# Optimization experiments

Measured on AMD Instinct MI355X. Metric: run time of the kernel, lower is better.

The kernel has to match this reference:

```python
import jax, jax.numpy as jnp
import numpy as np

N_SIN = 3  # fcn_n_sin

def _feats(x):
    # x: [B, Din] -> features [B, Din, 1 + 2*N_SIN]
    omega = (2.0 ** jnp.arange(N_SIN, dtype=x.dtype))  # [n_sin]
    ox = x[..., None] * omega  # [B, Din, n_sin]
    return jnp.concatenate([x[..., None], jnp.sin(ox), jnp.cos(ox)], axis=-1)

def setup_inputs() -> dict:
    key = jax.random.key(0)
    k1, k2, k3 = jax.random.split(key, 3)
    B, Din, Dout, H, F = 2048, 64, 64, 32, 1 + 2 * N_SIN
    x = jax.random.normal(k1, (B, Din), dtype=jnp.float32)
    # xavier-normal-ish init for W1/W2, zeros for biases (matches init_parameters)
    W1 = jax.random.normal(k2, (Din, Dout, H, F), dtype=jnp.float32) * np.sqrt(2.0 / (H + F))
    W2 = jax.random.normal(k3, (Din, Dout, 1, H), dtype=jnp.float32) * np.sqrt(2.0 / (1 + H))
    B1 = jnp.zeros((Din, Dout, H), dtype=jnp.float32)
    B2 = jnp.zeros((Din, Dout, 1), dtype=jnp.float32)
    return {"x": x, "W1": W1, "W2": W2, "B1": B1, "B2": B2}

def reference(x, W1, W2, B1, B2):
    f = _feats(x)  # [B, Din, F]
    # per-edge first layer: [B, Din, Dout, H]
    h = jnp.einsum('bif,iohf->bioh', f, W1) + B1[None]
    h = jax.nn.silu(h)
    # per-edge second layer -> scalar: [B, Din, Dout]
    phis = jnp.einsum('bioh,ioh->bio', h, W2[:, :, 0, :]) + B2[:, :, 0][None]
    return phis.sum(axis=1)  # [B, Dout]
```

## Files before the change

kernel.cpp:

```cpp
#include <hip/hip_runtime.h>
#include <math.h>

typedef _Float16 f16;
typedef f16   f16x8    __attribute__((ext_vector_type(8)));
typedef float floatx4  __attribute__((ext_vector_type(4)));
typedef float floatx16 __attribute__((ext_vector_type(16)));

#define LOG2E 1.44269504088896340736f

#define B_SZ  2048
#define DIN   64
#define DOUT  64
#define NH    32

#define NIG   2
#define IGW   (DIN / NIG)

#define W1IMG_ELEMS ((size_t)DIN * DOUT * 64 * 8)
#define FIMG_ELEMS  ((size_t)DIN * 64 * 64 * 8)
#define W2Q_ELEMS   ((size_t)DIN * DOUT * NH)

__global__ __launch_bounds__(256) void prep_kernel(
        const float* __restrict__ W1, const float* __restrict__ B1,
        const float* __restrict__ W2, const float* __restrict__ B2,
        const float* __restrict__ x,
        f16* __restrict__ w1img, f16* __restrict__ fimg,
        float* __restrict__ w2q, float* __restrict__ b2sum) {
    const int bid = blockIdx.x, tid = threadIdx.x;
    if (bid < 256) {
        __shared__ float l1[16 * 225];
        __shared__ float lb[16 * 32];
        const int base = bid * 16;
        for (int g = tid; g < 3584; g += 256) {
            int pair = g / 224, r = g % 224;
            l1[pair * 225 + r] = W1[(size_t)base * 224 + g];
        }
        for (int g = tid; g < 512; g += 256) lb[g] = B1[(size_t)base * 32 + g];
        __syncthreads();
        for (int g = tid; g < 1024; g += 256) {
            int pair = g >> 6, lane = g & 63;
            f16x8 v = {};
            if (lane < 32) {
#pragma unroll
                for (int j = 0; j < 7; ++j)
                    v[j] = (f16)(l1[pair * 225 + lane * 7 + j] * (-LOG2E));
                v[7] = (f16)(lb[pair * 32 + lane] * (-LOG2E));
            }
            *(f16x8*)(w1img + (size_t)bid * 8192 + (size_t)g * 8) = v;
        }
    } else if (bid < 320) {
        __shared__ float ls[32 * 65];
        const int btp = bid - 256;
        for (int g = tid; g < 2048; g += 256) {
            int bb = g >> 6, i = g & 63;
            ls[bb * 65 + i] = x[(size_t)(btp * 32 + bb) * 64 + i];
        }
        __syncthreads();
        for (int g = tid; g < 2048; g += 256) {
            int bb = g & 31, i = g >> 5;
            float xv = ls[bb * 65 + i];
            float s1, c1;
            __sincosf(xv, &s1, &c1);
            float s2 = 2.0f * s1 * c1, c2 = 1.0f - 2.0f * s1 * s1;
            float s4 = 2.0f * s2 * c2, c4 = 1.0f - 2.0f * s2 * s2;
            f16x8 v;
            v[0] = (f16)xv; v[1] = (f16)s1; v[2] = (f16)s2; v[3] = (f16)s4;
            v[4] = (f16)c1; v[5] = (f16)c2; v[6] = (f16)c4; v[7] = (f16)1.0f;
            *(f16x8*)(fimg + ((size_t)(i * 64 + btp) * 64 + bb) * 8) = v;
        }
    } else if (bid < 832) {
        int e = (bid - 320) * 256 + tid;
        int r = e & 3, p = (e >> 2) & 1, q = (e >> 3) & 3;
        int o = (e >> 5) & 63, i = e >> 11;
        int h = q * 8 + p * 4 + r;
        w2q[e] = W2[(size_t)(i * 64 + o) * 32 + h] * (-1.0f / LOG2E);
    } else if (tid < 64) {
        float s = 0.0f;
        for (int i = 0; i < 64; ++i) s += B2[i * 64 + tid];
        b2sum[tid] = s;
    }
}

__global__ __launch_bounds__(128, 4) void main_kernel(
        const f16* __restrict__ w1img, const f16* __restrict__ fimg,
        const float* __restrict__ w2q, float* __restrict__ partials) {
    const int tid  = threadIdx.x;
    const int lane = tid & 63;
    const int wv   = tid >> 6;
    const int btp  = blockIdx.x & 63;
    const int og   = (blockIdx.x >> 6) & 31;
    const int ig   = blockIdx.x >> 11;
    const int o    = __builtin_amdgcn_readfirstlane(og * 2 + wv);
    const int p    = lane >> 5;

    const size_t ibase = (size_t)ig * IGW;
    const f16*   ap = w1img + ibase * 32768 + ((size_t)o * 64 + lane) * 8;
    const f16*   bp = fimg  + ibase * 32768 + ((size_t)btp * 64 + lane) * 8;
    const float* wp = w2q   + ibase * 2048  + (size_t)o * 32 + p * 4;

    f16x8 a = *(const f16x8*)ap;
    f16x8 b = *(const f16x8*)bp;

    float phi = 0.0f;
    const floatx16 zeroC = {};

#pragma unroll 1
    for (int ii = 0; ii < IGW; ++ii) {
        const f16x8 ca = a, cb = b;

        const size_t i1 = (size_t)(ii + 1);
        a = *(const f16x8*)(ap + i1 * 32768);
        b = *(const f16x8*)(bp + i1 * 32768);

        const floatx4 w0 = *(const floatx4*)(wp + (size_t)ii * 2048);
        const floatx4 w1 = *(const floatx4*)(wp + (size_t)ii * 2048 + 8);
        const floatx4 w2 = *(const floatx4*)(wp + (size_t)ii * 2048 + 16);
        const floatx4 w3 = *(const floatx4*)(wp + (size_t)ii * 2048 + 24);

        floatx16 C = __builtin_amdgcn_mfma_f32_32x32x16_f16(ca, cb, zeroC, 0, 0, 0);

#pragma unroll
        for (int q = 0; q < 4; ++q) {
            const floatx4 wq = (q == 0) ? w0 : (q == 1) ? w1 : (q == 2) ? w2 : w3;
            float t0 = C[4 * q + 0], t1 = C[4 * q + 1];
            float t2 = C[4 * q + 2], t3 = C[4 * q + 3];
            float u0 = __builtin_amdgcn_exp2f(t0);
            float u1 = __builtin_amdgcn_exp2f(t1);
            float u2 = __builtin_amdgcn_exp2f(t2);
            float u3 = __builtin_amdgcn_exp2f(t3);
            float v0 = 1.0f + u0, v1 = 1.0f + u1, v2 = 1.0f + u2, v3 = 1.0f + u3;
            float p0 = t0 * wq[0], p1 = t1 * wq[1], p2 = t2 * wq[2], p3 = t3 * wq[3];
            float d01 = v0 * v1, d23 = v2 * v3;
            float n01 = __builtin_fmaf(p1, v0, p0 * v1);
            float n23 = __builtin_fmaf(p3, v2, p2 * v3);
            float n   = __builtin_fmaf(n23, d01, n01 * d23);
            float D   = d01 * d23;
            phi = __builtin_fmaf(n, __builtin_amdgcn_rcpf(D), phi);
        }
    }

    phi += __shfl_xor(phi, 32, 64);

    if (lane < 32) {
        partials[((size_t)ig * B_SZ + btp * 32 + lane) * 64 + o] = phi;
    }
}

__global__ __launch_bounds__(256) void reduce_kernel(
        const float* __restrict__ partials, const float* __restrict__ b2sum,
        float* __restrict__ out) {
    int t = blockIdx.x * 256 + threadIdx.x;
    floatx4 s = *(const floatx4*)(b2sum + ((t * 4) & 63));
#pragma unroll
    for (int gg = 0; gg < NIG; ++gg) {
        floatx4 v = *(const floatx4*)(partials + (size_t)gg * (B_SZ * DOUT) + t * 4);
        s += v;
    }
    *(floatx4*)(out + (size_t)t * 4) = s;
}

extern "C" void kernel_launch(void* const* d_in, const int* in_sizes, int n_in,
                              void* d_out, int out_size, void* d_ws, size_t ws_size,
                              hipStream_t stream) {
    const float* x  = (const float*)d_in[0];
    const float* W1 = (const float*)d_in[1];
    const float* W2 = (const float*)d_in[2];
    const float* B1 = (const float*)d_in[3];
    const float* B2 = (const float*)d_in[4];
    float* out = (float*)d_out;

    f16*   w1img    = (f16*)d_ws;
    f16*   fimg     = w1img + W1IMG_ELEMS;
    float* w2q      = (float*)(fimg + FIMG_ELEMS);
    float* b2sum    = w2q + W2Q_ELEMS;
    float* partials = b2sum + 64;

    prep_kernel<<<833, 256, 0, stream>>>(W1, B1, W2, B2, x, w1img, fimg, w2q, b2sum);
    main_kernel<<<NIG * 32 * 64, 128, 0, stream>>>(w1img, fimg, w2q, partials);
    reduce_kernel<<<(B_SZ * DOUT) / 1024, 256, 0, stream>>>(partials, b2sum, out);
}
```

Measured before the change: 131.5 us.

## Drop reduce kernel and W2 reorder; use atomics, split input dim finer

Removes the separate reduce kernel: the prep kernel now writes the B2 bias sum straight into the output, and the main kernel atomically adds its partial sums into it. The W2 reorder and prescale pass goes away: W2 is read directly and the -ln2 scale is applied once at the end. The input dimension is split into 4 groups instead of 2, and launch bounds allow 8 blocks per CU, to expose more parallelism. The SiLU epilogue now takes one reciprocal per element instead of combining four denominators before a single reciprocal, which adds transcendental work in exchange for fewer multiplies. The atomics make the summation order nondeterministic.

New measurement: 129.8 us. About the same (-1.3%).

```diff
diff --git a/kernel.cpp b/kernel.cpp
--- a/kernel.cpp
+++ b/kernel.cpp
@@ -7,25 +7,24 @@
 typedef float floatx16 __attribute__((ext_vector_type(16)));
 
 #define LOG2E 1.44269504088896340736f
+#define LN2   0.69314718055994530942f
 
 #define B_SZ  2048
 #define DIN   64
 #define DOUT  64
 #define NH    32
 
-#define NIG   2
+#define NIG   4
 #define IGW   (DIN / NIG)
 
 #define W1IMG_ELEMS ((size_t)DIN * DOUT * 64 * 8)
 #define FIMG_ELEMS  ((size_t)DIN * 64 * 64 * 8)
-#define W2Q_ELEMS   ((size_t)DIN * DOUT * NH)
 
 __global__ __launch_bounds__(256) void prep_kernel(
         const float* __restrict__ W1, const float* __restrict__ B1,
-        const float* __restrict__ W2, const float* __restrict__ B2,
-        const float* __restrict__ x,
+        const float* __restrict__ B2, const float* __restrict__ x,
         f16* __restrict__ w1img, f16* __restrict__ fimg,
-        float* __restrict__ w2q, float* __restrict__ b2sum) {
+        float* __restrict__ out) {
     const int bid = blockIdx.x, tid = threadIdx.x;
     if (bid < 256) {
         __shared__ float l1[16 * 225];
@@ -68,22 +67,19 @@
             v[4] = (f16)c1; v[5] = (f16)c2; v[6] = (f16)c4; v[7] = (f16)1.0f;
             *(f16x8*)(fimg + ((size_t)(i * 64 + btp) * 64 + bb) * 8) = v;
         }
-    } else if (bid < 832) {
+    } else {
         int e = (bid - 320) * 256 + tid;
-        int r = e & 3, p = (e >> 2) & 1, q = (e >> 3) & 3;
-        int o = (e >> 5) & 63, i = e >> 11;
-        int h = q * 8 + p * 4 + r;
-        w2q[e] = W2[(size_t)(i * 64 + o) * 32 + h] * (-1.0f / LOG2E);
-    } else if (tid < 64) {
+        int o = e & 63;
         float s = 0.0f;
-        for (int i = 0; i < 64; ++i) s += B2[i * 64 + tid];
-        b2sum[tid] = s;
+#pragma unroll 8
+        for (int i = 0; i < 64; ++i) s += B2[i * 64 + o];
+        out[e] = s;
     }
 }
 
-__global__ __launch_bounds__(128, 4) void main_kernel(
+__global__ __launch_bounds__(128, 8) void main_kernel(
         const f16* __restrict__ w1img, const f16* __restrict__ fimg,
-        const float* __restrict__ w2q, float* __restrict__ partials) {
+        const float* __restrict__ W2, float* __restrict__ out) {
     const int tid  = threadIdx.x;
     const int lane = tid & 63;
     const int wv   = tid >> 6;
@@ -96,7 +92,7 @@
     const size_t ibase = (size_t)ig * IGW;
     const f16*   ap = w1img + ibase * 32768 + ((size_t)o * 64 + lane) * 8;
     const f16*   bp = fimg  + ibase * 32768 + ((size_t)btp * 64 + lane) * 8;
-    const float* wp = w2q   + ibase * 2048  + (size_t)o * 32 + p * 4;
+    const float* wp = W2    + ibase * 2048  + (size_t)o * 32 + p * 4;
 
     f16x8 a = *(const f16x8*)ap;
     f16x8 b = *(const f16x8*)bp;
@@ -120,43 +116,29 @@
         floatx16 C = __builtin_amdgcn_mfma_f32_32x32x16_f16(ca, cb, zeroC, 0, 0, 0);
 
 #pragma unroll
-        for (int q = 0; q < 4; ++q) {
-            const floatx4 wq = (q == 0) ? w0 : (q == 1) ? w1 : (q == 2) ? w2 : w3;
-            float t0 = C[4 * q + 0], t1 = C[4 * q + 1];
-            float t2 = C[4 * q + 2], t3 = C[4 * q + 3];
-            float u0 = __builtin_amdgcn_exp2f(t0);
-            float u1 = __builtin_amdgcn_exp2f(t1);
-            float u2 = __builtin_amdgcn_exp2f(t2);
-            float u3 = __builtin_amdgcn_exp2f(t3);
-            float v0 = 1.0f + u0, v1 = 1.0f + u1, v2 = 1.0f + u2, v3 = 1.0f + u3;
-            float p0 = t0 * wq[0], p1 = t1 * wq[1], p2 = t2 * wq[2], p3 = t3 * wq[3];
-            float d01 = v0 * v1, d23 = v2 * v3;
-            float n01 = __builtin_fmaf(p1, v0, p0 * v1);
-            float n23 = __builtin_fmaf(p3, v2, p2 * v3);
-            float n   = __builtin_fmaf(n23, d01, n01 * d23);
-            float D   = d01 * d23;
-            phi = __builtin_fmaf(n, __builtin_amdgcn_rcpf(D), phi);
+        for (int r = 0; r < 4; ++r) {
+            float av, e2, sg;
+            av = C[0 + r];  e2 = __builtin_amdgcn_exp2f(av);
+            sg = __builtin_amdgcn_rcpf(1.0f + e2);
+            phi = __builtin_fmaf(av * w0[r], sg, phi);
+            av = C[4 + r];  e2 = __builtin_amdgcn_exp2f(av);
+            sg = __builtin_amdgcn_rcpf(1.0f + e2);
+            phi = __builtin_fmaf(av * w1[r], sg, phi);
+            av = C[8 + r];  e2 = __builtin_amdgcn_exp2f(av);
+            sg = __builtin_amdgcn_rcpf(1.0f + e2);
+            phi = __builtin_fmaf(av * w2[r], sg, phi);
+            av = C[12 + r]; e2 = __builtin_amdgcn_exp2f(av);
+            sg = __builtin_amdgcn_rcpf(1.0f + e2);
+            phi = __builtin_fmaf(av * w3[r], sg, phi);
         }
     }
 
     phi += __shfl_xor(phi, 32, 64);
+    phi *= -LN2;
 
     if (lane < 32) {
-        partials[((size_t)ig * B_SZ + btp * 32 + lane) * 64 + o] = phi;
+        atomicAdd(&out[(size_t)(btp * 32 + lane) * 64 + o], phi);
     }
-}
-
-__global__ __launch_bounds__(256) void reduce_kernel(
-        const float* __restrict__ partials, const float* __restrict__ b2sum,
-        float* __restrict__ out) {
-    int t = blockIdx.x * 256 + threadIdx.x;
-    floatx4 s = *(const floatx4*)(b2sum + ((t * 4) & 63));
-#pragma unroll
-    for (int gg = 0; gg < NIG; ++gg) {
-        floatx4 v = *(const floatx4*)(partials + (size_t)gg * (B_SZ * DOUT) + t * 4);
-        s += v;
-    }
-    *(floatx4*)(out + (size_t)t * 4) = s;
 }
 
 extern "C" void kernel_launch(void* const* d_in, const int* in_sizes, int n_in,
@@ -169,13 +151,9 @@
     const float* B2 = (const float*)d_in[4];
     float* out = (float*)d_out;
 
-    f16*   w1img    = (f16*)d_ws;
-    f16*   fimg     = w1img + W1IMG_ELEMS;
-    float* w2q      = (float*)(fimg + FIMG_ELEMS);
-    float* b2sum    = w2q + W2Q_ELEMS;
-    float* partials = b2sum + 64;
+    f16* w1img = (f16*)d_ws;
+    f16* fimg  = w1img + W1IMG_ELEMS;
 
-    prep_kernel<<<833, 256, 0, stream>>>(W1, B1, W2, B2, x, w1img, fimg, w2q, b2sum);
-    main_kernel<<<NIG * 32 * 64, 128, 0, stream>>>(w1img, fimg, w2q, partials);
-    reduce_kernel<<<(B_SZ * DOUT) / 1024, 256, 0, stream>>>(partials, b2sum, out);
+    prep_kernel<<<832, 256, 0, stream>>>(W1, B1, B2, x, w1img, fimg, out);
+    main_kernel<<<NIG * 32 * 64, 128, 0, stream>>>(w1img, fimg, W2, out);
 }
```
